# Performance work log

Measured on AMD Instinct MI355X. Metric: run time of the kernel, lower is better.

The kernel has to match this reference:

```python
import jax, jax.numpy as jnp
import numpy as np

B, S, D, H = 2, 2048, 1024, 16
HD = D // H          # 64
ROT = HD // 2        # 32

def _rope(x, cos, sin):
    # x: [B,S,H,HD] -> pairs [B,S,H,ROT,2]; cos/sin: [S,ROT] -> [1,S,1,ROT]
    x2 = x.reshape(x.shape[:3] + (ROT, 2))
    x0, x1 = x2[..., 0], x2[..., 1]
    c = cos[None, :, None, :]
    s = sin[None, :, None, :]
    out = jnp.stack([x0 * c - x1 * s, x1 * c + x0 * s], axis=-1)
    return out.reshape(x.shape)

def setup_inputs() -> dict:
    key = jax.random.key(0)
    ks = jax.random.split(key, 5)
    hidden_states = jax.random.normal(ks[0], (B, S, D), dtype=jnp.float32)
    # proper rotary cos/sin table: [S, ROT, 2]
    inv_freq = 1.0 / (10000.0 ** (np.arange(0, ROT, dtype=np.float32) / ROT))
    t = np.arange(S, dtype=np.float32)
    ang = np.outer(t, inv_freq)  # [S, ROT]
    freqs = jnp.asarray(np.stack([np.cos(ang), np.sin(ang)], axis=-1), dtype=jnp.float32)
    sc = 1.0 / np.sqrt(D)
    wq = jax.random.normal(ks[1], (D, D), dtype=jnp.float32) * sc
    wk = jax.random.normal(ks[2], (D, D), dtype=jnp.float32) * sc
    wv = jax.random.normal(ks[3], (D, D), dtype=jnp.float32) * sc
    wo = jax.random.normal(ks[4], (D, D), dtype=jnp.float32) * sc
    return {"hidden_states": hidden_states, "freqs": freqs, "wq": wq, "wk": wk, "wv": wv, "wo": wo}

def reference(hidden_states, freqs, wq, wk, wv, wo):
    b, s, _ = hidden_states.shape
    scaling = HD ** -0.5
    q = (hidden_states @ wq.T).reshape(b, s, H, HD)
    k = (hidden_states @ wk.T).reshape(b, s, H, HD)
    v = (hidden_states @ wv.T).reshape(b, s, H, HD)
    cos, sin = freqs[:s, :, 0], freqs[:s, :, 1]
    q = _rope(q, cos, sin)
    k = _rope(k, cos, sin)
    # [B,H,S,S] scores, fp32 softmax
    scores = jnp.einsum('bqhd,bkhd->bhqk', q, k) * scaling
    attn = jax.nn.softmax(scores.astype(jnp.float32), axis=-1).astype(q.dtype)
    out = jnp.einsum('bhqk,bkhd->bqhd', attn, v).reshape(b, s, D)
    return out @ wo.T
```

## Files before the change

kernel.cpp:

```cpp
#include <hip/hip_runtime.h>
#include <hip/hip_bf16.h>

typedef __attribute__((ext_vector_type(8))) short bf16x8;
typedef __attribute__((ext_vector_type(4))) float f32x4;
typedef __attribute__((ext_vector_type(16))) float f32x16;
typedef __attribute__((ext_vector_type(2))) float f32x2;
typedef unsigned short u16;

#define Bc   2
#define Sc   2048
#define Dc   1024
#define Hc   16
#define HDc  64
#define ROTc 32
#define Mrows 4096

__device__ __forceinline__ u16 f2bf(float x) {
  union { float f; unsigned u; } v{x};
  unsigned r = v.u + 0x7fffu + ((v.u >> 16) & 1u);
  return (u16)(r >> 16);
}
__device__ __forceinline__ float bf2f(u16 x) {
  union { unsigned u; float f; } v{(unsigned)x << 16};
  return v.f;
}
__device__ __forceinline__ unsigned cvtpk(float a, float b) {
  unsigned r;
  asm("v_cvt_pk_bf16_f32 %0, %1, %2" : "=v"(r) : "v"(a), "v"(b));
  return r;
}
__device__ __forceinline__ f32x2 pmax2(f32x2 a, f32x2 b) {
  f32x2 r;
  r.x = fmaxf(a.x, b.x);
  r.y = fmaxf(a.y, b.y);
  return r;
}

__device__ __forceinline__ void gload_lds16(const void* g, void* l) {
  __builtin_amdgcn_global_load_lds(
      (const __attribute__((address_space(1))) void*)g,
      (__attribute__((address_space(3))) void*)l, 16, 0, 0);
}

__global__ void cvt_all(const float* __restrict__ h, const float* __restrict__ q,
                        const float* __restrict__ k, const float* __restrict__ v,
                        const float* __restrict__ o,
                        u16* __restrict__ hb, u16* __restrict__ qb, u16* __restrict__ kb,
                        u16* __restrict__ vb, u16* __restrict__ ob) {
  size_t i = ((size_t)blockIdx.x * 256 + threadIdx.x) * 4;
  const float* s;
  u16* d;
  size_t off;
  if (i < (size_t)Mrows * Dc) {
    s = h; d = hb; off = i;
  } else {
    size_t j = i - (size_t)Mrows * Dc;
    int w = (int)(j >> 20);
    off = j & ((1u << 20) - 1);
    s = (w == 0) ? q : (w == 1) ? k : (w == 2) ? v : o;
    d = (w == 0) ? qb : (w == 1) ? kb : (w == 2) ? vb : ob;
  }
  float4 val = *reinterpret_cast<const float4*>(s + off);
  u16 r0 = f2bf(val.x), r1 = f2bf(val.y), r2 = f2bf(val.z), r3 = f2bf(val.w);
  ushort4 outv = {r0, r1, r2, r3};
  *reinterpret_cast<ushort4*>(d + off) = outv;
}

__global__ void gemm_qkv(const u16* __restrict__ A, const u16* __restrict__ W0,
                         const u16* __restrict__ W1, const u16* __restrict__ W2,
                         const float* __restrict__ freqs,
                         u16* __restrict__ Qo, u16* __restrict__ Ko,
                         u16* __restrict__ Vo) {
  __shared__ u16 As[128 * 32];
  __shared__ u16 Bs[128 * 32];
  const int orig = blockIdx.x;
  const int idx = orig >> 3;
  const int bx = (orig & 7) * 4 + (idx & 3);
  const int by = idx >> 2;
  const int wsel = by >> 3;
  const int n0 = (by & 7) * 128;
  const int m0 = bx * 128;
  const u16* Bm = (wsel == 0) ? W0 : (wsel == 1) ? W1 : W2;
  const int t = threadIdx.x;
  const int w = t >> 6;
  const int lane = t & 63;
  const int wm = w >> 1, wn = w & 1;
  const int c = lane & 15, g = lane >> 4;
  const int srow = t >> 2;
  const int skoff = ((t & 3) ^ (srow & 3)) * 8;

  f32x4 acc[4][4] = {};

  const u16* ag = A + (size_t)(m0 + srow) * Dc + skoff;
  const u16* bg = Bm + (size_t)(n0 + srow) * Dc + skoff;
  u16* al = &As[(w * 16) * 32];
  u16* bl = &Bs[(w * 16) * 32];

  for (int k0 = 0; k0 < Dc; k0 += 32) {
    gload_lds16(ag + k0, al);
    gload_lds16(ag + k0 + (size_t)64 * Dc, al + 64 * 32);
    gload_lds16(bg + k0, bl);
    gload_lds16(bg + k0 + (size_t)64 * Dc, bl + 64 * 32);
    __syncthreads();
    bf16x8 a[4], b[4];
#pragma unroll
    for (int f = 0; f < 4; ++f) {
      a[f] = *(const bf16x8*)&As[(wm * 64 + f * 16 + c) * 32 + (g ^ (c & 3)) * 8];
      b[f] = *(const bf16x8*)&Bs[(wn * 64 + f * 16 + c) * 32 + (g ^ (c & 3)) * 8];
    }
#pragma unroll
    for (int fm = 0; fm < 4; ++fm)
#pragma unroll
      for (int fn = 0; fn < 4; ++fn)
        acc[fm][fn] =
            __builtin_amdgcn_mfma_f32_16x16x32_bf16(a[fm], b[fn], acc[fm][fn], 0, 0, 0);
    __syncthreads();
  }

  u16* dst = (wsel == 0) ? Qo : (wsel == 1) ? Ko : Vo;
  const float qsc = (wsel == 0) ? 0.125f * 1.44269504f : 1.0f;
  const int codd = c & 1;
#pragma unroll
  for (int fm = 0; fm < 4; ++fm)
#pragma unroll
    for (int fn = 0; fn < 4; ++fn)
#pragma unroll
      for (int r = 0; r < 4; ++r) {
        const int m = m0 + wm * 64 + fm * 16 + g * 4 + r;
        const int n = n0 + wn * 64 + fn * 16 + c;
        float v = acc[fm][fn][r];
        const int b = m >> 11, s = m & (Sc - 1);
        const int hh = n >> 6, d = n & 63;
        size_t idx2;
        if (wsel < 2) {
          const float other = __shfl_xor(v, 1);
          const float2 f = reinterpret_cast<const float2*>(freqs)[s * ROTc + (d >> 1)];
          v = codd ? (v * f.x + other * f.y) : (v * f.x - other * f.y);
          v *= qsc;
          idx2 = (((size_t)(b * Hc + hh) * Sc) + s) * HDc + d;
        } else {
          idx2 = ((size_t)(b * Hc + hh) * HDc + d) * Sc + s;
        }
        dst[idx2] = f2bf(v);
      }
}

__global__ void gemm_out(const u16* __restrict__ A, const u16* __restrict__ Bm,
                         float* __restrict__ C) {
  __shared__ u16 As[64 * 32];
  __shared__ u16 Bs[128 * 32];
  const int m0 = blockIdx.x * 64;
  const int n0 = blockIdx.y * 128;
  const int t = threadIdx.x;
  const int w = t >> 6;
  const int lane = t & 63;
  const int wm = w >> 1, wn = w & 1;
  const int c = lane & 15, g = lane >> 4;
  const int srow = t >> 2;
  const int skoff = ((t & 3) ^ (srow & 3)) * 8;

  f32x4 acc[2][4] = {};

  const u16* ag = A + (size_t)(m0 + (srow & 63)) * Dc + skoff;
  const u16* bg = Bm + (size_t)(n0 + srow) * Dc + skoff;
  u16* al = &As[((t >> 2) & 63) * 0 + (w * 16) * 32];
  u16* bl = &Bs[(w * 16) * 32];

  for (int k0 = 0; k0 < Dc; k0 += 32) {
    gload_lds16(ag + k0, al);
    gload_lds16(bg + k0, bl);
    gload_lds16(bg + k0 + (size_t)64 * Dc, bl + 64 * 32);
    __syncthreads();
    bf16x8 a[2], b[4];
#pragma unroll
    for (int f = 0; f < 2; ++f)
      a[f] = *(const bf16x8*)&As[(wm * 32 + f * 16 + c) * 32 + (g ^ (c & 3)) * 8];
#pragma unroll
    for (int f = 0; f < 4; ++f)
      b[f] = *(const bf16x8*)&Bs[(wn * 64 + f * 16 + c) * 32 + (g ^ (c & 3)) * 8];
#pragma unroll
    for (int fm = 0; fm < 2; ++fm)
#pragma unroll
      for (int fn = 0; fn < 4; ++fn)
        acc[fm][fn] =
            __builtin_amdgcn_mfma_f32_16x16x32_bf16(a[fm], b[fn], acc[fm][fn], 0, 0, 0);
    __syncthreads();
  }

#pragma unroll
  for (int fm = 0; fm < 2; ++fm)
#pragma unroll
    for (int fn = 0; fn < 4; ++fn)
#pragma unroll
      for (int r = 0; r < 4; ++r) {
        const int m = m0 + wm * 32 + fm * 16 + g * 4 + r;
        const int n = n0 + wn * 64 + fn * 16 + c;
        C[(size_t)m * Dc + n] = acc[fm][fn][r];
      }
}

__global__ __launch_bounds__(512, 2) void flash_attn(
    const u16* __restrict__ Q, const u16* __restrict__ Kb,
    const u16* __restrict__ Vt, u16* __restrict__ Ob) {
  __shared__ u16 smem[18432];
  const int orig = blockIdx.x;
  const int wg = (orig & 7) * 64 + (orig >> 3);
  const int bh = wg >> 4;
  const int q0 = (wg & 15) * 128;
  const int t = threadIdx.x, w = t >> 6, lane = t & 63;
  const int grp = w >> 2, wl = w & 3;
  const int ts = t & 255;
  const int l31 = lane & 31, hi = lane >> 5;
  const int sr = ts >> 4;
  const int su = (ts & 15) ^ (sr & 15);
  const int skv = sr + ((su >> 3) << 5);
  const int sd8 = (su & 7) * 8;
  const int rsw = (l31 & 15);

  const u16* Qp = Q + (size_t)bh * Sc * HDc;
  const u16* Kp = Kb + (size_t)bh * Sc * HDc;
  const u16* Vp = Vt + (size_t)bh * HDc * Sc;
  u16* const Kg = smem + grp * 4096;
  u16* const Vg = smem + 8192 + grp * 4096;

  const int q = q0 + wl * 32 + l31;
  bf16x8 aq[4];
#pragma unroll
  for (int kd = 0; kd < 4; ++kd)
    aq[kd] = *(const bf16x8*)(Qp + (size_t)q * HDc + kd * 16 + hi * 8);

  float m_run = -1e30f, l_run = 0.f;
  f32x16 o0 = {}, o1 = {};

  auto STAGE = [&](int tile) {
    const int base = grp * 1024 + tile * 64;
    gload_lds16(Kp + (size_t)(base + skv) * HDc + sd8, Kg + wl * 512);
    gload_lds16(Kp + (size_t)(base + skv + 16) * HDc + sd8, Kg + 2048 + wl * 512);
    gload_lds16(Vp + (size_t)skv * Sc + base + sd8, Vg + wl * 512);
    gload_lds16(Vp + (size_t)(skv + 16) * Sc + base + sd8, Vg + 2048 + wl * 512);
  };

  for (int tt = 0; tt < 16; ++tt) {
    STAGE(tt);
    __syncthreads();
    f32x16 s0 = {}, s1 = {};
    __builtin_amdgcn_s_setprio(1);
#pragma unroll
    for (int kd = 0; kd < 4; ++kd) {
      const int u0 = kd * 2 + hi;
      bf16x8 a0 = *(const bf16x8*)&Kg[l31 * 128 + (u0 ^ rsw) * 8];
      bf16x8 a1 = *(const bf16x8*)&Kg[l31 * 128 + ((u0 + 8) ^ rsw) * 8];
      s0 = __builtin_amdgcn_mfma_f32_32x32x16_bf16(a0, aq[kd], s0, 0, 0, 0);
      s1 = __builtin_amdgcn_mfma_f32_32x32x16_bf16(a1, aq[kd], s1, 0, 0, 0);
    }
    __builtin_amdgcn_s_setprio(0);
    f32x2 t4[4];
#pragma unroll
    for (int i = 0; i < 4; ++i) {
      f32x2 e0; e0.x = s0[2 * i]; e0.y = s0[2 * i + 1];
      f32x2 e1; e1.x = s0[2 * i + 8]; e1.y = s0[2 * i + 9];
      f32x2 e2; e2.x = s1[2 * i]; e2.y = s1[2 * i + 1];
      f32x2 e3; e3.x = s1[2 * i + 8]; e3.y = s1[2 * i + 9];
      t4[i] = pmax2(pmax2(e0, e1), pmax2(e2, e3));
    }
    f32x2 tp = pmax2(pmax2(t4[0], t4[1]), pmax2(t4[2], t4[3]));
    float mt = fmaxf(tp.x, tp.y);
    mt = fmaxf(mt, __shfl_xor(mt, 32));
    const bool skip = __all(mt <= m_run + 8.0f);
    if (!skip) {
      const float mn2 = fmaxf(m_run, mt);
      const float scl = __builtin_amdgcn_exp2f(m_run - mn2);
      m_run = mn2;
      l_run *= scl;
      o0 *= scl;
      o1 *= scl;
    }
    const float mn = m_run;
#pragma unroll
    for (int r = 0; r < 16; ++r) {
      s0[r] = __builtin_amdgcn_exp2f(s0[r] - mn);
      s1[r] = __builtin_amdgcn_exp2f(s1[r] - mn);
    }
    f32x2 ac;
    ac.x = 0.f; ac.y = 0.f;
#pragma unroll
    for (int i = 0; i < 8; ++i) {
      f32x2 e0; e0.x = s0[2 * i]; e0.y = s0[2 * i + 1];
      f32x2 e1; e1.x = s1[2 * i]; e1.y = s1[2 * i + 1];
      ac += e0 + e1;
    }
    float rs = ac.x + ac.y;
    rs += __shfl_xor(rs, 32);
    l_run += rs;
    unsigned pk0[8], pk1[8];
#pragma unroll
    for (int B = 0; B < 4; ++B)
#pragma unroll
      for (int s2 = 0; s2 < 2; ++s2) {
        pk0[B * 2 + s2] = cvtpk(s0[4 * B + 2 * s2], s0[4 * B + 2 * s2 + 1]);
        pk1[B * 2 + s2] = cvtpk(s1[4 * B + 2 * s2], s1[4 * B + 2 * s2 + 1]);
      }
#pragma unroll
    for (int ks = 0; ks < 4; ++ks) {
      const unsigned* pk = (ks >> 1) ? pk1 : pk0;
      const int m2 = (ks & 1) * 4;
      const unsigned A0 = pk[m2 + 0], A1 = pk[m2 + 1];
      const unsigned B0 = pk[m2 + 2], B1 = pk[m2 + 3];
      const unsigned L0 = hi ? B0 : A0, L1 = hi ? B1 : A1;
      const unsigned R0 = hi ? A0 : B0, R1 = hi ? A1 : B1;
      const unsigned X0 = __shfl_xor(R0, 32), X1 = __shfl_xor(R1, 32);
      union { unsigned u[4]; bf16x8 v; } bp;
      bp.u[0] = hi ? X0 : L0;
      bp.u[1] = hi ? X1 : L1;
      bp.u[2] = hi ? L0 : X0;
      bp.u[3] = hi ? L1 : X1;
      const int uv = ks * 2 + hi;
      bf16x8 va0 = *(const bf16x8*)&Vg[l31 * 128 + (uv ^ rsw) * 8];
      bf16x8 va1 = *(const bf16x8*)&Vg[l31 * 128 + ((uv + 8) ^ rsw) * 8];
      __builtin_amdgcn_s_setprio(1);
      o0 = __builtin_amdgcn_mfma_f32_32x32x16_bf16(va0, bp.v, o0, 0, 0, 0);
      o1 = __builtin_amdgcn_mfma_f32_32x32x16_bf16(va1, bp.v, o1, 0, 0, 0);
      __builtin_amdgcn_s_setprio(0);
    }
    __syncthreads();
  }

  float* fl = reinterpret_cast<float*>(smem);
  const int slot = (wl * 64 + lane) * 34;
  if (grp == 1) {
#pragma unroll
    for (int j = 0; j < 16; ++j) fl[slot + j] = o0[j];
#pragma unroll
    for (int j = 0; j < 16; ++j) fl[slot + 16 + j] = o1[j];
    fl[slot + 32] = m_run;
    fl[slot + 33] = l_run;
  }
  __syncthreads();
  if (grp == 0) {
    const float mB = fl[slot + 32], lB = fl[slot + 33];
    const float mx = fmaxf(m_run, mB);
    const float sA = __builtin_amdgcn_exp2f(m_run - mx);
    const float sB = __builtin_amdgcn_exp2f(mB - mx);
    const float rd = 1.0f / (l_run * sA + lB * sB);
    const float cA = sA * rd, cB = sB * rd;
    const int b = bh >> 4, hh = bh & 15;
    u16* orow = Ob + ((size_t)b * Sc + q) * Dc + hh * HDc;
#pragma unroll
    for (int B2 = 0; B2 < 4; ++B2) {
      const float v0 = o0[4 * B2 + 0] * cA + fl[slot + 4 * B2 + 0] * cB;
      const float v1 = o0[4 * B2 + 1] * cA + fl[slot + 4 * B2 + 1] * cB;
      const float v2 = o0[4 * B2 + 2] * cA + fl[slot + 4 * B2 + 2] * cB;
      const float v3 = o0[4 * B2 + 3] * cA + fl[slot + 4 * B2 + 3] * cB;
      uint2 pv;
      pv.x = cvtpk(v0, v1);
      pv.y = cvtpk(v2, v3);
      *reinterpret_cast<uint2*>(orow + 8 * B2 + 4 * hi) = pv;
    }
#pragma unroll
    for (int B2 = 0; B2 < 4; ++B2) {
      const float v0 = o1[4 * B2 + 0] * cA + fl[slot + 16 + 4 * B2 + 0] * cB;
      const float v1 = o1[4 * B2 + 1] * cA + fl[slot + 16 + 4 * B2 + 1] * cB;
      const float v2 = o1[4 * B2 + 2] * cA + fl[slot + 16 + 4 * B2 + 2] * cB;
      const float v3 = o1[4 * B2 + 3] * cA + fl[slot + 16 + 4 * B2 + 3] * cB;
      uint2 pv;
      pv.x = cvtpk(v0, v1);
      pv.y = cvtpk(v2, v3);
      *reinterpret_cast<uint2*>(orow + 32 + 8 * B2 + 4 * hi) = pv;
    }
  }
}

extern "C" void kernel_launch(void* const* d_in, const int* in_sizes, int n_in,
                              void* d_out, int out_size, void* d_ws, size_t ws_size,
                              hipStream_t stream) {
  (void)in_sizes; (void)n_in; (void)out_size; (void)ws_size;
  const float* hidden = (const float*)d_in[0];
  const float* freqs = (const float*)d_in[1];
  const float* wq = (const float*)d_in[2];
  const float* wk = (const float*)d_in[3];
  const float* wv = (const float*)d_in[4];
  const float* wo = (const float*)d_in[5];
  float* out = (float*)d_out;

  char* ws = (char*)d_ws;
  const size_t MB8 = (size_t)Mrows * Dc * 2;
  const size_t WB = (size_t)Dc * Dc * 2;
  u16* hb = (u16*)ws;  ws += MB8;
  u16* wqb = (u16*)ws; ws += WB;
  u16* wkb = (u16*)ws; ws += WB;
  u16* wvb = (u16*)ws; ws += WB;
  u16* wob = (u16*)ws; ws += WB;
  u16* qb = (u16*)ws;  ws += MB8;
  u16* kb = (u16*)ws;  ws += MB8;
  u16* vtb = (u16*)ws; ws += MB8;
  u16* ab = (u16*)ws;  ws += MB8;

  cvt_all<<<8192, 256, 0, stream>>>(hidden, wq, wk, wv, wo, hb, wqb, wkb, wvb, wob);
  gemm_qkv<<<768, 256, 0, stream>>>(hb, wqb, wkb, wvb, freqs, qb, kb, vtb);
  flash_attn<<<512, 512, 0, stream>>>(qb, kb, vtb, ab);
  gemm_out<<<dim3(64, 8), 256, 0, stream>>>(ab, wob, out);
}
```

Before: 128.5 us.

## Fuse Q/K/V projections into one block sharing A tiles with double-buffered LDS

The QKV projection kernel now computes all three weight outputs in each block, reusing each loaded activation tile across Q, K and V instead of loading it three times. The grid drops from 768 to 256 blocks. It adds double-buffered LDS staging, so the next k-slice loads while the current one is multiplied, and raises wave priority around the MFMA section. The cost is three times as many accumulator registers (192 floats per lane) and a much larger LDS footprint, which lowers occupancy, and the smaller grid may underfill the CUs.

After: 131.4 us. 1.02x slower.

```diff
diff --git a/kernel.cpp b/kernel.cpp
--- a/kernel.cpp
+++ b/kernel.cpp
@@ -66,21 +66,15 @@
   *reinterpret_cast<ushort4*>(d + off) = outv;
 }
 
-__global__ void gemm_qkv(const u16* __restrict__ A, const u16* __restrict__ W0,
-                         const u16* __restrict__ W1, const u16* __restrict__ W2,
-                         const float* __restrict__ freqs,
-                         u16* __restrict__ Qo, u16* __restrict__ Ko,
-                         u16* __restrict__ Vo) {
-  __shared__ u16 As[128 * 32];
-  __shared__ u16 Bs[128 * 32];
-  const int orig = blockIdx.x;
-  const int idx = orig >> 3;
-  const int bx = (orig & 7) * 4 + (idx & 3);
-  const int by = idx >> 2;
-  const int wsel = by >> 3;
-  const int n0 = (by & 7) * 128;
-  const int m0 = bx * 128;
-  const u16* Bm = (wsel == 0) ? W0 : (wsel == 1) ? W1 : W2;
+__global__ __launch_bounds__(256) void gemm_qkv3(
+    const u16* __restrict__ A, const u16* __restrict__ W0,
+    const u16* __restrict__ W1, const u16* __restrict__ W2,
+    const float* __restrict__ freqs,
+    u16* __restrict__ Qo, u16* __restrict__ Ko, u16* __restrict__ Vo) {
+  __shared__ u16 As[2 * 4096];
+  __shared__ u16 Bs[2 * 3 * 4096];
+  const int m0 = blockIdx.x * 128;
+  const int n0 = blockIdx.y * 128;
   const int t = threadIdx.x;
   const int w = t >> 6;
   const int lane = t & 63;
@@ -89,36 +83,84 @@
   const int srow = t >> 2;
   const int skoff = ((t & 3) ^ (srow & 3)) * 8;
 
-  f32x4 acc[4][4] = {};
+  f32x4 accq[4][4] = {};
+  f32x4 acck[4][4] = {};
+  f32x4 accv[4][4] = {};
 
   const u16* ag = A + (size_t)(m0 + srow) * Dc + skoff;
-  const u16* bg = Bm + (size_t)(n0 + srow) * Dc + skoff;
-  u16* al = &As[(w * 16) * 32];
-  u16* bl = &Bs[(w * 16) * 32];
-
+  const u16* bg0 = W0 + (size_t)(n0 + srow) * Dc + skoff;
+  const u16* bg1 = W1 + (size_t)(n0 + srow) * Dc + skoff;
+  const u16* bg2 = W2 + (size_t)(n0 + srow) * Dc + skoff;
+  const int ldst = w * 512;
+
+  auto STAGE = [&](int k0, int bb) {
+    gload_lds16(ag + k0, &As[bb * 4096 + ldst]);
+    gload_lds16(ag + k0 + (size_t)64 * Dc, &As[bb * 4096 + 2048 + ldst]);
+    gload_lds16(bg0 + k0, &Bs[bb * 12288 + ldst]);
+    gload_lds16(bg0 + k0 + (size_t)64 * Dc, &Bs[bb * 12288 + 2048 + ldst]);
+    gload_lds16(bg1 + k0, &Bs[bb * 12288 + 4096 + ldst]);
+    gload_lds16(bg1 + k0 + (size_t)64 * Dc, &Bs[bb * 12288 + 6144 + ldst]);
+    gload_lds16(bg2 + k0, &Bs[bb * 12288 + 8192 + ldst]);
+    gload_lds16(bg2 + k0 + (size_t)64 * Dc, &Bs[bb * 12288 + 10240 + ldst]);
+  };
+
+  STAGE(0, 0);
+  __syncthreads();
+
+  int buf = 0;
   for (int k0 = 0; k0 < Dc; k0 += 32) {
-    gload_lds16(ag + k0, al);
-    gload_lds16(ag + k0 + (size_t)64 * Dc, al + 64 * 32);
-    gload_lds16(bg + k0, bl);
-    gload_lds16(bg + k0 + (size_t)64 * Dc, bl + 64 * 32);
+    if (k0 + 32 < Dc) STAGE(k0 + 32, buf ^ 1);
+    bf16x8 a[4];
+#pragma unroll
+    for (int f = 0; f < 4; ++f)
+      a[f] = *(const bf16x8*)&As[buf * 4096 + (wm * 64 + f * 16 + c) * 32 +
+                                 (g ^ (c & 3)) * 8];
+    __builtin_amdgcn_s_setprio(1);
+    {
+      bf16x8 b[4];
+#pragma unroll
+      for (int f = 0; f < 4; ++f)
+        b[f] = *(const bf16x8*)&Bs[buf * 12288 + (wn * 64 + f * 16 + c) * 32 +
+                                   (g ^ (c & 3)) * 8];
+#pragma unroll
+      for (int fm = 0; fm < 4; ++fm)
+#pragma unroll
+        for (int fn = 0; fn < 4; ++fn)
+          accq[fm][fn] =
+              __builtin_amdgcn_mfma_f32_16x16x32_bf16(a[fm], b[fn], accq[fm][fn], 0, 0, 0);
+    }
+    {
+      bf16x8 b[4];
+#pragma unroll
+      for (int f = 0; f < 4; ++f)
+        b[f] = *(const bf16x8*)&Bs[buf * 12288 + 4096 + (wn * 64 + f * 16 + c) * 32 +
+                                   (g ^ (c & 3)) * 8];
+#pragma unroll
+      for (int fm = 0; fm < 4; ++fm)
+#pragma unroll
+        for (int fn = 0; fn < 4; ++fn)
+          acck[fm][fn] =
+              __builtin_amdgcn_mfma_f32_16x16x32_bf16(a[fm], b[fn], acck[fm][fn], 0, 0, 0);
+    }
+    {
+      bf16x8 b[4];
+#pragma unroll
+      for (int f = 0; f < 4; ++f)
+        b[f] = *(const bf16x8*)&Bs[buf * 12288 + 8192 + (wn * 64 + f * 16 + c) * 32 +
+                                   (g ^ (c & 3)) * 8];
+#pragma unroll
+      for (int fm = 0; fm < 4; ++fm)
+#pragma unroll
+        for (int fn = 0; fn < 4; ++fn)
+          accv[fm][fn] =
+              __builtin_amdgcn_mfma_f32_16x16x32_bf16(a[fm], b[fn], accv[fm][fn], 0, 0, 0);
+    }
+    __builtin_amdgcn_s_setprio(0);
     __syncthreads();
-    bf16x8 a[4], b[4];
-#pragma unroll
-    for (int f = 0; f < 4; ++f) {
-      a[f] = *(const bf16x8*)&As[(wm * 64 + f * 16 + c) * 32 + (g ^ (c & 3)) * 8];
-      b[f] = *(const bf16x8*)&Bs[(wn * 64 + f * 16 + c) * 32 + (g ^ (c & 3)) * 8];
-    }
-#pragma unroll
-    for (int fm = 0; fm < 4; ++fm)
-#pragma unroll
-      for (int fn = 0; fn < 4; ++fn)
-        acc[fm][fn] =
-            __builtin_amdgcn_mfma_f32_16x16x32_bf16(a[fm], b[fn], acc[fm][fn], 0, 0, 0);
-    __syncthreads();
-  }
-
-  u16* dst = (wsel == 0) ? Qo : (wsel == 1) ? Ko : Vo;
-  const float qsc = (wsel == 0) ? 0.125f * 1.44269504f : 1.0f;
+    buf ^= 1;
+  }
+
+  const float qsc = 0.125f * 1.44269504f;
   const int codd = c & 1;
 #pragma unroll
   for (int fm = 0; fm < 4; ++fm)
@@ -128,20 +170,42 @@
       for (int r = 0; r < 4; ++r) {
         const int m = m0 + wm * 64 + fm * 16 + g * 4 + r;
         const int n = n0 + wn * 64 + fn * 16 + c;
-        float v = acc[fm][fn][r];
+        float v = accq[fm][fn][r];
         const int b = m >> 11, s = m & (Sc - 1);
         const int hh = n >> 6, d = n & 63;
-        size_t idx2;
-        if (wsel < 2) {
-          const float other = __shfl_xor(v, 1);
-          const float2 f = reinterpret_cast<const float2*>(freqs)[s * ROTc + (d >> 1)];
-          v = codd ? (v * f.x + other * f.y) : (v * f.x - other * f.y);
-          v *= qsc;
-          idx2 = (((size_t)(b * Hc + hh) * Sc) + s) * HDc + d;
-        } else {
-          idx2 = ((size_t)(b * Hc + hh) * HDc + d) * Sc + s;
-        }
-        dst[idx2] = f2bf(v);
+        const float other = __shfl_xor(v, 1);
+        const float2 f = reinterpret_cast<const float2*>(freqs)[s * ROTc + (d >> 1)];
+        v = codd ? (v * f.x + other * f.y) : (v * f.x - other * f.y);
+        v *= qsc;
+        Qo[(((size_t)(b * Hc + hh) * Sc) + s) * HDc + d] = f2bf(v);
+      }
+#pragma unroll
+  for (int fm = 0; fm < 4; ++fm)
+#pragma unroll
+    for (int fn = 0; fn < 4; ++fn)
+#pragma unroll
+      for (int r = 0; r < 4; ++r) {
+        const int m = m0 + wm * 64 + fm * 16 + g * 4 + r;
+        const int n = n0 + wn * 64 + fn * 16 + c;
+        float v = acck[fm][fn][r];
+        const int b = m >> 11, s = m & (Sc - 1);
+        const int hh = n >> 6, d = n & 63;
+        const float other = __shfl_xor(v, 1);
+        const float2 f = reinterpret_cast<const float2*>(freqs)[s * ROTc + (d >> 1)];
+        v = codd ? (v * f.x + other * f.y) : (v * f.x - other * f.y);
+        Ko[(((size_t)(b * Hc + hh) * Sc) + s) * HDc + d] = f2bf(v);
+      }
+#pragma unroll
+  for (int fm = 0; fm < 4; ++fm)
+#pragma unroll
+    for (int fn = 0; fn < 4; ++fn)
+#pragma unroll
+      for (int r = 0; r < 4; ++r) {
+        const int m = m0 + wm * 64 + fm * 16 + g * 4 + r;
+        const int n = n0 + wn * 64 + fn * 16 + c;
+        const int b = m >> 11, s = m & (Sc - 1);
+        const int hh = n >> 6, d = n & 63;
+        Vo[((size_t)(b * Hc + hh) * HDc + d) * Sc + s] = f2bf(accv[fm][fn][r]);
       }
 }
 
@@ -163,7 +227,7 @@
 
   const u16* ag = A + (size_t)(m0 + (srow & 63)) * Dc + skoff;
   const u16* bg = Bm + (size_t)(n0 + srow) * Dc + skoff;
-  u16* al = &As[((t >> 2) & 63) * 0 + (w * 16) * 32];
+  u16* al = &As[(w * 16) * 32];
   u16* bl = &Bs[(w * 16) * 32];
 
   for (int k0 = 0; k0 < Dc; k0 += 32) {
@@ -396,7 +460,7 @@
   u16* ab = (u16*)ws;  ws += MB8;
 
   cvt_all<<<8192, 256, 0, stream>>>(hidden, wq, wk, wv, wo, hb, wqb, wkb, wvb, wob);
-  gemm_qkv<<<768, 256, 0, stream>>>(hb, wqb, wkb, wvb, freqs, qb, kb, vtb);
+  gemm_qkv3<<<dim3(32, 8), 256, 0, stream>>>(hb, wqb, wkb, wvb, freqs, qb, kb, vtb);
   flash_attn<<<512, 512, 0, stream>>>(qb, kb, vtb, ab);
   gemm_out<<<dim3(64, 8), 256, 0, stream>>>(ab, wob, out);
 }
```

## Double GEMM K-tile to 64 with 8-way swizzle, setprio, and plain 2D grid

Applied to the files above, without the earlier changes.

Both projection GEMMs now stage 64-wide K tiles in LDS instead of 32, with an 8-chunk XOR swizzle. This halves the number of barrier pairs per K loop and issues more loads per stage. The MFMA bursts are wrapped in s_setprio to favour the math waves. The QKV GEMM drops its grouped block-index remap in favour of a plain 2D grid, which may change L2 reuse. LDS use doubles, which could limit occupancy.

New measurement: 126.8 us, median of 2. Within noise of the previous version (-1.3%).

```diff
diff --git a/kernel.cpp b/kernel.cpp
--- a/kernel.cpp
+++ b/kernel.cpp
@@ -71,49 +71,54 @@
                          const float* __restrict__ freqs,
                          u16* __restrict__ Qo, u16* __restrict__ Ko,
                          u16* __restrict__ Vo) {
-  __shared__ u16 As[128 * 32];
-  __shared__ u16 Bs[128 * 32];
-  const int orig = blockIdx.x;
-  const int idx = orig >> 3;
-  const int bx = (orig & 7) * 4 + (idx & 3);
-  const int by = idx >> 2;
+  __shared__ u16 As[128 * 64];
+  __shared__ u16 Bs[128 * 64];
+  const int by = blockIdx.y;
   const int wsel = by >> 3;
   const int n0 = (by & 7) * 128;
-  const int m0 = bx * 128;
+  const int m0 = blockIdx.x * 128;
   const u16* Bm = (wsel == 0) ? W0 : (wsel == 1) ? W1 : W2;
   const int t = threadIdx.x;
   const int w = t >> 6;
   const int lane = t & 63;
   const int wm = w >> 1, wn = w & 1;
   const int c = lane & 15, g = lane >> 4;
-  const int srow = t >> 2;
-  const int skoff = ((t & 3) ^ (srow & 3)) * 8;
+  const int sr = t >> 3;
+  const int skoff = ((t & 7) ^ (sr & 7)) * 8;
 
   f32x4 acc[4][4] = {};
 
-  const u16* ag = A + (size_t)(m0 + srow) * Dc + skoff;
-  const u16* bg = Bm + (size_t)(n0 + srow) * Dc + skoff;
-  u16* al = &As[(w * 16) * 32];
-  u16* bl = &Bs[(w * 16) * 32];
-
-  for (int k0 = 0; k0 < Dc; k0 += 32) {
-    gload_lds16(ag + k0, al);
-    gload_lds16(ag + k0 + (size_t)64 * Dc, al + 64 * 32);
-    gload_lds16(bg + k0, bl);
-    gload_lds16(bg + k0 + (size_t)64 * Dc, bl + 64 * 32);
-    __syncthreads();
-    bf16x8 a[4], b[4];
-#pragma unroll
-    for (int f = 0; f < 4; ++f) {
-      a[f] = *(const bf16x8*)&As[(wm * 64 + f * 16 + c) * 32 + (g ^ (c & 3)) * 8];
-      b[f] = *(const bf16x8*)&Bs[(wn * 64 + f * 16 + c) * 32 + (g ^ (c & 3)) * 8];
-    }
-#pragma unroll
-    for (int fm = 0; fm < 4; ++fm)
-#pragma unroll
-      for (int fn = 0; fn < 4; ++fn)
-        acc[fm][fn] =
-            __builtin_amdgcn_mfma_f32_16x16x32_bf16(a[fm], b[fn], acc[fm][fn], 0, 0, 0);
+  const u16* ag = A + (size_t)(m0 + sr) * Dc + skoff;
+  const u16* bg = Bm + (size_t)(n0 + sr) * Dc + skoff;
+  const int ldst = w * 512;
+
+  for (int k0 = 0; k0 < Dc; k0 += 64) {
+#pragma unroll
+    for (int site = 0; site < 4; ++site) {
+      gload_lds16(ag + k0 + (size_t)(site * 32) * Dc, &As[site * 2048 + ldst]);
+      gload_lds16(bg + k0 + (size_t)(site * 32) * Dc, &Bs[site * 2048 + ldst]);
+    }
+    __syncthreads();
+#pragma unroll
+    for (int sub = 0; sub < 2; ++sub) {
+      bf16x8 a[4], b[4];
+#pragma unroll
+      for (int f = 0; f < 4; ++f) {
+        const int row = wm * 64 + f * 16 + c;
+        const int p = ((sub * 4 + g) ^ (c & 7)) * 8;
+        a[f] = *(const bf16x8*)&As[row * 64 + p];
+        const int rowb = wn * 64 + f * 16 + c;
+        b[f] = *(const bf16x8*)&Bs[rowb * 64 + p];
+      }
+      __builtin_amdgcn_s_setprio(1);
+#pragma unroll
+      for (int fm = 0; fm < 4; ++fm)
+#pragma unroll
+        for (int fn = 0; fn < 4; ++fn)
+          acc[fm][fn] =
+              __builtin_amdgcn_mfma_f32_16x16x32_bf16(a[fm], b[fn], acc[fm][fn], 0, 0, 0);
+      __builtin_amdgcn_s_setprio(0);
+    }
     __syncthreads();
   }
 
@@ -147,8 +152,8 @@
 
 __global__ void gemm_out(const u16* __restrict__ A, const u16* __restrict__ Bm,
                          float* __restrict__ C) {
-  __shared__ u16 As[64 * 32];
-  __shared__ u16 Bs[128 * 32];
+  __shared__ u16 As[64 * 64];
+  __shared__ u16 Bs[128 * 64];
   const int m0 = blockIdx.x * 64;
   const int n0 = blockIdx.y * 128;
   const int t = threadIdx.x;
@@ -156,34 +161,42 @@
   const int lane = t & 63;
   const int wm = w >> 1, wn = w & 1;
   const int c = lane & 15, g = lane >> 4;
-  const int srow = t >> 2;
-  const int skoff = ((t & 3) ^ (srow & 3)) * 8;
+  const int sr = t >> 3;
+  const int skoff = ((t & 7) ^ (sr & 7)) * 8;
 
   f32x4 acc[2][4] = {};
 
-  const u16* ag = A + (size_t)(m0 + (srow & 63)) * Dc + skoff;
-  const u16* bg = Bm + (size_t)(n0 + srow) * Dc + skoff;
-  u16* al = &As[((t >> 2) & 63) * 0 + (w * 16) * 32];
-  u16* bl = &Bs[(w * 16) * 32];
-
-  for (int k0 = 0; k0 < Dc; k0 += 32) {
-    gload_lds16(ag + k0, al);
-    gload_lds16(bg + k0, bl);
-    gload_lds16(bg + k0 + (size_t)64 * Dc, bl + 64 * 32);
-    __syncthreads();
-    bf16x8 a[2], b[4];
-#pragma unroll
-    for (int f = 0; f < 2; ++f)
-      a[f] = *(const bf16x8*)&As[(wm * 32 + f * 16 + c) * 32 + (g ^ (c & 3)) * 8];
-#pragma unroll
-    for (int f = 0; f < 4; ++f)
-      b[f] = *(const bf16x8*)&Bs[(wn * 64 + f * 16 + c) * 32 + (g ^ (c & 3)) * 8];
-#pragma unroll
-    for (int fm = 0; fm < 2; ++fm)
-#pragma unroll
-      for (int fn = 0; fn < 4; ++fn)
-        acc[fm][fn] =
-            __builtin_amdgcn_mfma_f32_16x16x32_bf16(a[fm], b[fn], acc[fm][fn], 0, 0, 0);
+  const u16* ag = A + (size_t)(m0 + sr) * Dc + skoff;
+  const u16* bg = Bm + (size_t)(n0 + sr) * Dc + skoff;
+  const int ldst = w * 512;
+
+  for (int k0 = 0; k0 < Dc; k0 += 64) {
+#pragma unroll
+    for (int site = 0; site < 2; ++site)
+      gload_lds16(ag + k0 + (size_t)(site * 32) * Dc, &As[site * 2048 + ldst]);
+#pragma unroll
+    for (int site = 0; site < 4; ++site)
+      gload_lds16(bg + k0 + (size_t)(site * 32) * Dc, &Bs[site * 2048 + ldst]);
+    __syncthreads();
+#pragma unroll
+    for (int sub = 0; sub < 2; ++sub) {
+      bf16x8 a[2], b[4];
+      const int p = ((sub * 4 + g) ^ (c & 7)) * 8;
+#pragma unroll
+      for (int f = 0; f < 2; ++f)
+        a[f] = *(const bf16x8*)&As[(wm * 32 + f * 16 + c) * 64 + p];
+#pragma unroll
+      for (int f = 0; f < 4; ++f)
+        b[f] = *(const bf16x8*)&Bs[(wn * 64 + f * 16 + c) * 64 + p];
+      __builtin_amdgcn_s_setprio(1);
+#pragma unroll
+      for (int fm = 0; fm < 2; ++fm)
+#pragma unroll
+        for (int fn = 0; fn < 4; ++fn)
+          acc[fm][fn] =
+              __builtin_amdgcn_mfma_f32_16x16x32_bf16(a[fm], b[fn], acc[fm][fn], 0, 0, 0);
+      __builtin_amdgcn_s_setprio(0);
+    }
     __syncthreads();
   }
 
@@ -396,7 +409,7 @@
   u16* ab = (u16*)ws;  ws += MB8;
 
   cvt_all<<<8192, 256, 0, stream>>>(hidden, wq, wk, wv, wo, hb, wqb, wkb, wvb, wob);
-  gemm_qkv<<<768, 256, 0, stream>>>(hb, wqb, wkb, wvb, freqs, qb, kb, vtb);
+  gemm_qkv<<<dim3(32, 24), 256, 0, stream>>>(hb, wqb, wkb, wvb, freqs, qb, kb, vtb);
   flash_attn<<<512, 512, 0, stream>>>(qb, kb, vtb, ab);
   gemm_out<<<dim3(64, 8), 256, 0, stream>>>(ab, wob, out);
 }
```
